# Optimization experiments

Measured on AMD Instinct MI355X. Metric: run time of the kernel, lower is better.

Reference implementation:

```python
import jax, jax.numpy as jnp
import numpy as np


def setup_inputs() -> dict:
    key = jax.random.key(0)
    ks = jax.random.split(key, 6)
    B, L, NC = 32, 10000, 80
    REG_MAX, K, HID = 32, 4, 64
    IN = 4 * (K + 1)  # 20
    scores = jax.random.normal(ks[0], (B, L, NC), dtype=jnp.float32)
    pred_corners = jax.random.normal(ks[1], (B, L, 4 * (REG_MAX + 1)), dtype=jnp.float32)
    w1 = jax.random.normal(ks[2], (HID, IN), dtype=jnp.float32) * (1.0 / np.sqrt(IN))
    b1 = jax.random.normal(ks[3], (HID,), dtype=jnp.float32) * 0.01
    w2 = jax.random.normal(ks[4], (1, HID), dtype=jnp.float32) * (1.0 / np.sqrt(HID))
    b2 = jax.random.normal(ks[5], (1,), dtype=jnp.float32) * 0.01
    return {"scores": scores, "pred_corners": pred_corners,
            "w1": w1, "b1": b1, "w2": w2, "b2": b2, "k_top": K}


def reference(scores, pred_corners, w1, b1, w2, b2, k_top):
    B, L, D = pred_corners.shape
    nbins = D // 4  # reg_max + 1
    # softmax over the distribution bins of each of the 4 box sides
    prob = jax.nn.softmax(pred_corners.reshape(B, L, 4, nbins), axis=-1)
    prob_topk, _ = jax.lax.top_k(prob, k_top)                      # [B, L, 4, k]
    stat = jnp.concatenate(
        [prob_topk, prob_topk.mean(axis=-1, keepdims=True)], axis=-1)  # [B, L, 4, k+1]
    stat = stat.reshape(B, L, 4 * (k_top + 1))                     # [B, L, 4*(k+1)]
    # tiny MLP: Linear -> ReLU -> Linear
    h = jax.nn.relu(jnp.einsum('bli,hi->blh', stat, w1) + b1)      # [B, L, hid]
    quality = jnp.einsum('blh,oh->blo', h, w2) + b2                # [B, L, 1]
    return scores + quality
```

## Files before the change

### kernel.cpp

```cpp
#include <hip/hip_runtime.h>
#include <cmath>


constexpr int NB   = 33;
constexpr int NS   = 4;
constexpr int DPR  = 132;
constexpr int HID  = 64;
constexpr int NCLS = 80;
constexpr int APB  = 256;

__global__ __launch_bounds__(APB, 4) void lqe_fused(
    const float* __restrict__ scores,
    const float* __restrict__ pred,
    const float* __restrict__ w1,
    const float* __restrict__ b1,
    const float* __restrict__ w2,
    const float* __restrict__ b2,
    float* __restrict__ out)
{
    __shared__ float s_x[APB * NB];
    __shared__ float s_w1[20 * HID];
    __shared__ float s_b1[HID];
    __shared__ float s_w2[HID];
    __shared__ float s_b2;

    const int t = threadIdx.x;
    const long long ab = (long long)blockIdx.x * APB;

    for (int i = t; i < 20 * HID; i += APB) {
        int j  = i & (HID - 1);
        int sq = i >> 6;
        s_w1[i] = w1[j * 20 + sq];
    }
    if (t < HID) { s_b1[t] = b1[t]; s_w2[t] = w2[t]; }
    if (t == 0)  { s_b2 = b2[0]; }

    float h[HID];
    #pragma unroll
    for (int j = 0; j < HID; ++j) h[j] = 0.0f;

    for (int s = 0; s < NS; ++s) {
        __syncthreads();
        const float* src = pred + ab * DPR + s * NB;
        #pragma unroll 1
        for (int i = t; i < APB * NB; i += APB) {
            int a = i / NB;
            int j = i - a * NB;
            s_x[i] = src[a * DPR + j];
        }
        __syncthreads();

        float x[NB];
        #pragma unroll
        for (int j = 0; j < NB; ++j) x[j] = s_x[t * NB + j];

        float t0 = -INFINITY, t1 = -INFINITY, t2 = -INFINITY, t3 = -INFINITY;
        #pragma unroll
        for (int j = 0; j < NB; ++j) {
            float v  = x[j];
            float n0 = fminf(t0, v);  t0 = fmaxf(t0, v);
            float n1 = fminf(t1, n0); t1 = fmaxf(t1, n0);
            float n2 = fminf(t2, n1); t2 = fmaxf(t2, n1);
            t3 = fmaxf(t3, n2);
        }

        float sum = 0.0f;
        #pragma unroll
        for (int j = 0; j < NB; ++j) sum += __expf(x[j] - t0);
        float inv = 1.0f / sum;

        float f0 = inv;
        float f1 = __expf(t1 - t0) * inv;
        float f2 = __expf(t2 - t0) * inv;
        float f3 = __expf(t3 - t0) * inv;
        float fm = 0.25f * (f0 + f1 + f2 + f3);
        float f[5] = {f0, f1, f2, f3, fm};

        const float* wb = &s_w1[s * 5 * HID];
        #pragma unroll
        for (int q = 0; q < 5; ++q) {
            float fq = f[q];
            const float4* wq = (const float4*)(wb + q * HID);
            #pragma unroll
            for (int j4 = 0; j4 < HID / 4; ++j4) {
                float4 w = wq[j4];
                h[4*j4+0] = fmaf(fq, w.x, h[4*j4+0]);
                h[4*j4+1] = fmaf(fq, w.y, h[4*j4+1]);
                h[4*j4+2] = fmaf(fq, w.z, h[4*j4+2]);
                h[4*j4+3] = fmaf(fq, w.w, h[4*j4+3]);
            }
        }
    }

    float qv = s_b2;
    #pragma unroll
    for (int j = 0; j < HID; ++j) {
        float hv = fmaxf(h[j] + s_b1[j], 0.0f);
        qv = fmaf(hv, s_w2[j], qv);
    }

    __syncthreads();
    s_x[t] = qv;
    __syncthreads();

    const float4* sc4 = (const float4*)(scores + ab * NCLS);
    float4*       ot4 = (float4*)(out + ab * NCLS);
    #pragma unroll 1
    for (int i = t; i < APB * NCLS / 4; i += APB) {
        float q = s_x[i / 20];
        float4 v = sc4[i];
        v.x += q; v.y += q; v.z += q; v.w += q;
        ot4[i] = v;
    }
}

extern "C" void kernel_launch(void* const* d_in, const int* in_sizes, int n_in,
                              void* d_out, int out_size, void* d_ws, size_t ws_size,
                              hipStream_t stream) {
    const float* scores = (const float*)d_in[0];
    const float* pred   = (const float*)d_in[1];
    const float* w1     = (const float*)d_in[2];
    const float* b1     = (const float*)d_in[3];
    const float* w2     = (const float*)d_in[4];
    const float* b2     = (const float*)d_in[5];

    int n_anchor = in_sizes[0] / NCLS;
    int blocks   = n_anchor / APB;
    lqe_fused<<<blocks, APB, 0, stream>>>(scores, pred, w1, b1, w2, b2,
                                          (float*)d_out);
}
```

Before: 413.3 us.

## Fold mean into weights, read pred rows directly, and drop the shared staging buffer

Folds the top-k mean term into the first-layer weights, which shrinks the MLP input from 20 to 16 features. Each thread now reads its own anchor's 132 logits straight from global memory as float4 loads, so the shared-memory staging buffer and the per-side block barriers are gone. Top-4 selection is done on exponentiated values without max subtraction. This lowers LDS use and synchronisation, but each thread's loads are strided by a 528-byte row, so global accesses across a wave are uncoalesced. Unshifted exp could also overflow for large logits.

```diff
diff --git a/kernel.cpp b/kernel.cpp
--- a/kernel.cpp
+++ b/kernel.cpp
@@ -3,7 +3,6 @@
 
 
 constexpr int NB   = 33;
-constexpr int NS   = 4;
 constexpr int DPR  = 132;
 constexpr int HID  = 64;
 constexpr int NCLS = 80;
@@ -18,76 +17,50 @@
     const float* __restrict__ b2,
     float* __restrict__ out)
 {
-    __shared__ float s_x[APB * NB];
-    __shared__ float s_w1[20 * HID];
+    __shared__ float s_w1[HID * 16];
     __shared__ float s_b1[HID];
     __shared__ float s_w2[HID];
     __shared__ float s_b2;
+    __shared__ float s_q[APB];
 
     const int t = threadIdx.x;
     const long long ab = (long long)blockIdx.x * APB;
 
-    for (int i = t; i < 20 * HID; i += APB) {
-        int j  = i & (HID - 1);
-        int sq = i >> 6;
-        s_w1[i] = w1[j * 20 + sq];
+    for (int i = t; i < HID * 16; i += APB) {
+        int j = i >> 4, col = i & 15;
+        int s = col >> 2, q = col & 3;
+        s_w1[i] = w1[j * 20 + s * 5 + q] + 0.25f * w1[j * 20 + s * 5 + 4];
     }
     if (t < HID) { s_b1[t] = b1[t]; s_w2[t] = w2[t]; }
     if (t == 0)  { s_b2 = b2[0]; }
+    __syncthreads();
 
-    float h[HID];
+    const float4* pp = (const float4*)(pred + (ab + t) * (long long)DPR);
+
+    float f[16];
+    float e0 = 0.f, e1 = 0.f, e2 = 0.f, e3 = 0.f, sum = 0.f;
+
     #pragma unroll
-    for (int j = 0; j < HID; ++j) h[j] = 0.0f;
-
-    for (int s = 0; s < NS; ++s) {
-        __syncthreads();
-        const float* src = pred + ab * DPR + s * NB;
-        #pragma unroll 1
-        for (int i = t; i < APB * NB; i += APB) {
-            int a = i / NB;
-            int j = i - a * NB;
-            s_x[i] = src[a * DPR + j];
-        }
-        __syncthreads();
-
-        float x[NB];
+    for (int ld = 0; ld < 33; ++ld) {
+        float4 v = pp[ld];
+        float vv[4] = {v.x, v.y, v.z, v.w};
         #pragma unroll
-        for (int j = 0; j < NB; ++j) x[j] = s_x[t * NB + j];
-
-        float t0 = -INFINITY, t1 = -INFINITY, t2 = -INFINITY, t3 = -INFINITY;
-        #pragma unroll
-        for (int j = 0; j < NB; ++j) {
-            float v  = x[j];
-            float n0 = fminf(t0, v);  t0 = fmaxf(t0, v);
-            float n1 = fminf(t1, n0); t1 = fmaxf(t1, n0);
-            float n2 = fminf(t2, n1); t2 = fmaxf(t2, n1);
-            t3 = fmaxf(t3, n2);
-        }
-
-        float sum = 0.0f;
-        #pragma unroll
-        for (int j = 0; j < NB; ++j) sum += __expf(x[j] - t0);
-        float inv = 1.0f / sum;
-
-        float f0 = inv;
-        float f1 = __expf(t1 - t0) * inv;
-        float f2 = __expf(t2 - t0) * inv;
-        float f3 = __expf(t3 - t0) * inv;
-        float fm = 0.25f * (f0 + f1 + f2 + f3);
-        float f[5] = {f0, f1, f2, f3, fm};
-
-        const float* wb = &s_w1[s * 5 * HID];
-        #pragma unroll
-        for (int q = 0; q < 5; ++q) {
-            float fq = f[q];
-            const float4* wq = (const float4*)(wb + q * HID);
-            #pragma unroll
-            for (int j4 = 0; j4 < HID / 4; ++j4) {
-                float4 w = wq[j4];
-                h[4*j4+0] = fmaf(fq, w.x, h[4*j4+0]);
-                h[4*j4+1] = fmaf(fq, w.y, h[4*j4+1]);
-                h[4*j4+2] = fmaf(fq, w.z, h[4*j4+2]);
-                h[4*j4+3] = fmaf(fq, w.w, h[4*j4+3]);
+        for (int c = 0; c < 4; ++c) {
+            const int idx = 4 * ld + c;
+            float e = __expf(vv[c]);
+            sum += e;
+            float n0 = fminf(e0, e);  e0 = fmaxf(e0, e);
+            float n1 = fminf(e1, n0); e1 = fmaxf(e1, n0);
+            float n2 = fminf(e2, n1); e2 = fmaxf(e2, n1);
+            e3 = fmaxf(e3, n2);
+            if (idx % NB == NB - 1) {
+                const int s = idx / NB;
+                float inv = 1.0f / sum;
+                f[s * 4 + 0] = e0 * inv;
+                f[s * 4 + 1] = e1 * inv;
+                f[s * 4 + 2] = e2 * inv;
+                f[s * 4 + 3] = e3 * inv;
+                e0 = e1 = e2 = e3 = 0.f; sum = 0.f;
             }
         }
     }
@@ -95,19 +68,28 @@
     float qv = s_b2;
     #pragma unroll
     for (int j = 0; j < HID; ++j) {
-        float hv = fmaxf(h[j] + s_b1[j], 0.0f);
-        qv = fmaf(hv, s_w2[j], qv);
+        const float4* wr = (const float4*)(s_w1 + j * 16);
+        float hj = s_b1[j];
+        #pragma unroll
+        for (int i4 = 0; i4 < 4; ++i4) {
+            float4 w = wr[i4];
+            hj = fmaf(f[4 * i4 + 0], w.x, hj);
+            hj = fmaf(f[4 * i4 + 1], w.y, hj);
+            hj = fmaf(f[4 * i4 + 2], w.z, hj);
+            hj = fmaf(f[4 * i4 + 3], w.w, hj);
+        }
+        hj = fmaxf(hj, 0.f);
+        qv = fmaf(hj, s_w2[j], qv);
     }
 
-    __syncthreads();
-    s_x[t] = qv;
+    s_q[t] = qv;
     __syncthreads();
 
     const float4* sc4 = (const float4*)(scores + ab * NCLS);
     float4*       ot4 = (float4*)(out + ab * NCLS);
     #pragma unroll 1
     for (int i = t; i < APB * NCLS / 4; i += APB) {
-        float q = s_x[i / 20];
+        float q = s_q[i / 20];
         float4 v = sc4[i];
         v.x += q; v.y += q; v.z += q; v.w += q;
         ot4[i] = v;
```

Measured after the change: 353.8 us. 1.17x faster.
